# Kernel optimization log

Hardware: AMD Instinct MI355X
Metric: run time of the kernel (lower is better)

The kernel has to match this reference:

```python
import jax, jax.numpy as jnp
import numpy as np

TEMPERATURE = 2.0  # registered buffer in the torch module
TAU = 1.0
N_HEADS = 16


def setup_inputs() -> dict:
    key = jax.random.key(0)
    ks = jax.random.split(key, 8)
    B, S, D, N = 4, 1024, 1024, 4096
    scale = 1.0 / np.sqrt(D)
    return {
        "x": jax.random.normal(ks[0], (B, S, D), jnp.float32),
        "in_proj_w": jax.random.normal(ks[1], (3 * D, D), jnp.float32) * scale,
        "in_proj_b": jnp.zeros((3 * D,), jnp.float32),
        "out_w": jax.random.normal(ks[2], (D, D), jnp.float32) * scale,
        "out_b": jnp.zeros((D,), jnp.float32),
        "aff_w": jax.random.normal(ks[3], (N, D), jnp.float32) * scale,
        "aff_b": jnp.zeros((N,), jnp.float32),
        "k": 256,
    }


def _forward(x, in_proj_w, in_proj_b, out_w, out_b, aff_w, aff_b, k):
    B, S, D = x.shape
    H = N_HEADS
    hd = D // H
    # packed QKV projection (torch nn.MultiheadAttention layout)
    qkv = x @ in_proj_w.T + in_proj_b                      # [B,S,3D]
    q, kk, v = jnp.split(qkv, 3, axis=-1)
    q = q.reshape(B, S, H, hd).transpose(0, 2, 1, 3)       # [B,H,S,hd]
    kk = kk.reshape(B, S, H, hd).transpose(0, 2, 1, 3)
    v = v.reshape(B, S, H, hd).transpose(0, 2, 1, 3)
    scores = jnp.einsum("bhqd,bhkd->bhqk", q, kk) / np.sqrt(hd)
    attn = jax.nn.softmax(scores, axis=-1)                 # [B,H,S,S]
    ctx = jnp.einsum("bhqk,bhkd->bhqd", attn, v)
    ctx = ctx.transpose(0, 2, 1, 3).reshape(B, S, D)
    context = ctx @ out_w.T + out_b                        # [B,S,D]
    # neuron affinity -> max-pool over sequence
    affinity = context @ aff_w.T + aff_b                   # [B,S,N]
    pooled = affinity.max(axis=1)                          # [B,N]
    logits = pooled / TEMPERATURE
    # eval path of gumbel-softmax-topk: plain softmax(logits / tau)
    soft = jax.nn.softmax(logits / TAU, axis=-1)
    _, idx = jax.lax.top_k(logits, k)                      # [B,k]
    mask = jnp.zeros_like(soft).at[jnp.arange(soft.shape[0])[:, None], idx].set(1.0)
    masked = soft * mask
    weights = masked / (masked.sum(axis=-1, keepdims=True) + 1e-8)
    return idx, weights, context


def reference(x, in_proj_w, in_proj_b, out_w, out_b, aff_w, aff_b, k):
    return _forward(x, in_proj_w, in_proj_b, out_w, out_b, aff_w, aff_b, k)
```

## Files before the change

### kernel.cpp

```cpp
#include <hip/hip_runtime.h>
#include <math.h>

namespace {

constexpr int Bb = 4, Ss = 1024, Dd = 1024, Hh = 16, HDim = 64, Nn = 4096;
constexpr int Mm = Bb * Ss;

template <int MODE, int TM>
__global__ __launch_bounds__(256, 2) void gemm_f32(
    const float* __restrict__ A, const float* __restrict__ W,
    const float* __restrict__ bias, float* __restrict__ C, const int K,
    const int ldc) {
  constexpr int BM = TM * 16;
  __shared__ float As[2][16][BM];
  __shared__ float Ws[2][16][128];
  __shared__ float red[2][128];
  const int tid = threadIdx.x;
  const int lane = tid & 63, wv = tid >> 6;
  const int wm = wv >> 1, wn = wv & 1;
  const int lty = lane >> 3, ltx = lane & 7;
  const int m0 = blockIdx.y * BM, n0 = blockIdx.x * 128;
  const int row0 = wm * (BM / 2) + lty * TM;
  const int col0 = wn * 64 + ltx * 8;
  const int asrow = (TM == 8) ? (tid >> 1) : (tid >> 2);
  const int asoff = (TM == 8) ? ((tid & 1) * 8) : ((tid & 3) * 4);
  const int bsrow = tid >> 1, bsoff = (tid & 1) * 8;
  const float* Ap = A + (size_t)(m0 + asrow) * K + asoff;
  const float* Wp = W + (size_t)(n0 + bsrow) * K + bsoff;

  float4 a0r, a1r, w0r, w1r;
  a0r = *(const float4*)(Ap);
  if constexpr (TM == 8) a1r = *(const float4*)(Ap + 4);
  w0r = *(const float4*)(Wp);
  w1r = *(const float4*)(Wp + 4);

  float acc[TM][8] = {};
  const int NT = K / 16;
#pragma unroll 1
  for (int kt = 0; kt < NT; ++kt) {
    float* Ab = &As[kt & 1][0][0];
    float* Wb = &Ws[kt & 1][0][0];
    Ab[(asoff + 0) * BM + asrow] = a0r.x;
    Ab[(asoff + 1) * BM + asrow] = a0r.y;
    Ab[(asoff + 2) * BM + asrow] = a0r.z;
    Ab[(asoff + 3) * BM + asrow] = a0r.w;
    if constexpr (TM == 8) {
      Ab[(asoff + 4) * BM + asrow] = a1r.x;
      Ab[(asoff + 5) * BM + asrow] = a1r.y;
      Ab[(asoff + 6) * BM + asrow] = a1r.z;
      Ab[(asoff + 7) * BM + asrow] = a1r.w;
    }
    Wb[(bsoff + 0) * 128 + bsrow] = w0r.x;
    Wb[(bsoff + 1) * 128 + bsrow] = w0r.y;
    Wb[(bsoff + 2) * 128 + bsrow] = w0r.z;
    Wb[(bsoff + 3) * 128 + bsrow] = w0r.w;
    Wb[(bsoff + 4) * 128 + bsrow] = w1r.x;
    Wb[(bsoff + 5) * 128 + bsrow] = w1r.y;
    Wb[(bsoff + 6) * 128 + bsrow] = w1r.z;
    Wb[(bsoff + 7) * 128 + bsrow] = w1r.w;
    __syncthreads();
    if (kt + 1 < NT) {
      const int kb = (kt + 1) * 16;
      a0r = *(const float4*)(Ap + kb);
      if constexpr (TM == 8) a1r = *(const float4*)(Ap + kb + 4);
      w0r = *(const float4*)(Wp + kb);
      w1r = *(const float4*)(Wp + kb + 4);
    }
#pragma unroll
    for (int kk = 0; kk < 16; ++kk) {
      float4 aq0 = *(const float4*)&Ab[kk * BM + row0];
      float4 aq1;
      if constexpr (TM == 8) aq1 = *(const float4*)&Ab[kk * BM + row0 + 4];
      float4 bq0 = *(const float4*)&Wb[kk * 128 + col0];
      float4 bq1 = *(const float4*)&Wb[kk * 128 + col0 + 4];
      float av[TM];
      av[0] = aq0.x; av[1] = aq0.y; av[2] = aq0.z; av[3] = aq0.w;
      if constexpr (TM == 8) {
        av[4] = aq1.x; av[5] = aq1.y; av[6] = aq1.z; av[7] = aq1.w;
      }
      const float bv[8] = {bq0.x, bq0.y, bq0.z, bq0.w,
                           bq1.x, bq1.y, bq1.z, bq1.w};
#pragma unroll
      for (int i = 0; i < TM; ++i)
#pragma unroll
        for (int j = 0; j < 8; ++j)
          acc[i][j] = fmaf(av[i], bv[j], acc[i][j]);
    }
  }

  if constexpr (MODE == 0) {
    float4 bb0 = *(const float4*)&bias[n0 + col0];
    float4 bb1 = *(const float4*)&bias[n0 + col0 + 4];
    const float bvv[8] = {bb0.x, bb0.y, bb0.z, bb0.w,
                          bb1.x, bb1.y, bb1.z, bb1.w};
#pragma unroll
    for (int i = 0; i < TM; ++i) {
      float* crow = C + (size_t)(m0 + row0 + i) * ldc + n0 + col0;
      float4 o0 = {acc[i][0] + bvv[0], acc[i][1] + bvv[1],
                   acc[i][2] + bvv[2], acc[i][3] + bvv[3]};
      float4 o1 = {acc[i][4] + bvv[4], acc[i][5] + bvv[5],
                   acc[i][6] + bvv[6], acc[i][7] + bvv[7]};
      *(float4*)(crow) = o0;
      *(float4*)(crow + 4) = o1;
    }
  } else {
    float cm[8];
#pragma unroll
    for (int j = 0; j < 8; ++j) {
      float m = acc[0][j];
#pragma unroll
      for (int i = 1; i < TM; ++i) m = fmaxf(m, acc[i][j]);
      m = fmaxf(m, __shfl_xor(m, 8));
      m = fmaxf(m, __shfl_xor(m, 16));
      m = fmaxf(m, __shfl_xor(m, 32));
      cm[j] = m;
    }
    __syncthreads();
    if (lty == 0) {
      float4 c0 = {cm[0], cm[1], cm[2], cm[3]};
      float4 c1 = {cm[4], cm[5], cm[6], cm[7]};
      *(float4*)&red[wm][wn * 64 + ltx * 8] = c0;
      *(float4*)&red[wm][wn * 64 + ltx * 8 + 4] = c1;
    }
    __syncthreads();
    if (tid < 128)
      C[(size_t)blockIdx.y * ldc + n0 + tid] =
          fmaxf(red[0][tid], red[1][tid]);
  }
}

__device__ __forceinline__ int swz(int r, int c) {
  return c ^ ((((r >> 3) ^ r) & 7) << 2);
}

__global__ __launch_bounds__(64, 1) void attn_kernel(
    const float* __restrict__ qkv, float* __restrict__ ctx) {
  __shared__ float Qs[64][64];
  __shared__ float KP[32 * 64];
  __shared__ float Vs[32][64];
  const int lane = threadIdx.x;
  const int rg = lane >> 3, cg = lane & 7;
  const int id = blockIdx.x;
  const int qt = id >> 6, bh = id & 63;
  const int b = bh >> 4, h = bh & 15;
  const int q0 = qt * 64;
  const size_t rstride = 3 * Dd;
  const float* qb = qkv + (size_t)b * Ss * rstride + h * HDim;
  const float* kb_ = qb + Dd;
  const float* vb_ = qb + 2 * Dd;
  {
    const float* qr = qb + (size_t)(q0 + lane) * rstride;
#pragma unroll
    for (int c = 0; c < 64; c += 4)
      *(float4*)&Qs[lane][swz(lane, c)] = *(const float4*)(qr + c);
  }
  const int krow = lane >> 1, khalf = (lane & 1) * 32;
  float4 kreg[8], vreg[8];
  {
    const float* kp = kb_ + (size_t)krow * rstride + khalf;
    const float* vp = vb_ + (size_t)krow * rstride + khalf;
#pragma unroll
    for (int c = 0; c < 8; ++c) {
      kreg[c] = *(const float4*)(kp + 4 * c);
      vreg[c] = *(const float4*)(vp + 4 * c);
    }
  }
  float O[8][8] = {};
  float mr[8], lr[8];
#pragma unroll
  for (int i = 0; i < 8; ++i) { mr[i] = -INFINITY; lr[i] = 0.f; }

#pragma unroll 1
  for (int kt = 0; kt < Ss; kt += 32) {
#pragma unroll
    for (int c = 0; c < 8; ++c) {
      *(float4*)&KP[krow * 64 + swz(krow, khalf + 4 * c)] = kreg[c];
      *(float4*)&Vs[krow][swz(krow, khalf + 4 * c)] = vreg[c];
    }
    if (kt + 32 < Ss) {
      const float* kp = kb_ + (size_t)(kt + 32 + krow) * rstride + khalf;
      const float* vp = vb_ + (size_t)(kt + 32 + krow) * rstride + khalf;
#pragma unroll
      for (int c = 0; c < 8; ++c) {
        kreg[c] = *(const float4*)(kp + 4 * c);
        vreg[c] = *(const float4*)(vp + 4 * c);
      }
    }
    float sc[8][4] = {};
#pragma unroll
    for (int d0 = 0; d0 < HDim; d0 += 4) {
      float4 qa[8], kv[4];
#pragma unroll
      for (int i = 0; i < 8; ++i) {
        const int r = rg * 8 + i;
        qa[i] = *(const float4*)&Qs[r][swz(r, d0)];
      }
#pragma unroll
      for (int j = 0; j < 4; ++j) {
        const int r = cg * 4 + j;
        kv[j] = *(const float4*)&KP[r * 64 + swz(r, d0)];
      }
#pragma unroll
      for (int i = 0; i < 8; ++i)
#pragma unroll
        for (int j = 0; j < 4; ++j) {
          sc[i][j] = fmaf(qa[i].x, kv[j].x, sc[i][j]);
          sc[i][j] = fmaf(qa[i].y, kv[j].y, sc[i][j]);
          sc[i][j] = fmaf(qa[i].z, kv[j].z, sc[i][j]);
          sc[i][j] = fmaf(qa[i].w, kv[j].w, sc[i][j]);
        }
    }
#pragma unroll
    for (int i = 0; i < 8; ++i) {
      const float s0 = sc[i][0] * 0.125f, s1 = sc[i][1] * 0.125f;
      const float s2 = sc[i][2] * 0.125f, s3 = sc[i][3] * 0.125f;
      float tm = fmaxf(fmaxf(s0, s1), fmaxf(s2, s3));
      tm = fmaxf(tm, __shfl_xor(tm, 1));
      tm = fmaxf(tm, __shfl_xor(tm, 2));
      tm = fmaxf(tm, __shfl_xor(tm, 4));
      const float mnew = fmaxf(mr[i], tm);
      const float p0 = __expf(s0 - mnew), p1 = __expf(s1 - mnew);
      const float p2 = __expf(s2 - mnew), p3 = __expf(s3 - mnew);
      float rs = p0 + p1 + p2 + p3;
      rs += __shfl_xor(rs, 1);
      rs += __shfl_xor(rs, 2);
      rs += __shfl_xor(rs, 4);
      const float corr = __expf(mr[i] - mnew);
      lr[i] = lr[i] * corr + rs;
      mr[i] = mnew;
#pragma unroll
      for (int c = 0; c < 8; ++c) O[i][c] *= corr;
      const int r = rg * 8 + i;
      float4 pv = {p0, p1, p2, p3};
      *(float4*)&KP[r * 32 + swz(r, cg * 4)] = pv;
    }
#pragma unroll
    for (int k0 = 0; k0 < 32; k0 += 4) {
      float4 pa[8];
#pragma unroll
      for (int i = 0; i < 8; ++i) {
        const int r = rg * 8 + i;
        pa[i] = *(const float4*)&KP[r * 32 + swz(r, k0)];
      }
#pragma unroll
      for (int jj = 0; jj < 4; ++jj) {
        const int vr = k0 + jj;
        const float4 v0 = *(const float4*)&Vs[vr][swz(vr, cg * 8)];
        const float4 v1 = *(const float4*)&Vs[vr][swz(vr, cg * 8 + 4)];
#pragma unroll
        for (int i = 0; i < 8; ++i) {
          const float p = (jj == 0) ? pa[i].x
                          : (jj == 1) ? pa[i].y
                          : (jj == 2) ? pa[i].z : pa[i].w;
          O[i][0] = fmaf(p, v0.x, O[i][0]);
          O[i][1] = fmaf(p, v0.y, O[i][1]);
          O[i][2] = fmaf(p, v0.z, O[i][2]);
          O[i][3] = fmaf(p, v0.w, O[i][3]);
          O[i][4] = fmaf(p, v1.x, O[i][4]);
          O[i][5] = fmaf(p, v1.y, O[i][5]);
          O[i][6] = fmaf(p, v1.z, O[i][6]);
          O[i][7] = fmaf(p, v1.w, O[i][7]);
        }
      }
    }
  }
#pragma unroll
  for (int i = 0; i < 8; ++i) {
    const float inv = 1.0f / lr[i];
    float* orow =
        ctx + ((size_t)(b * Ss + q0 + rg * 8 + i)) * Dd + h * HDim + cg * 8;
    float4 o0 = {O[i][0] * inv, O[i][1] * inv, O[i][2] * inv, O[i][3] * inv};
    float4 o1 = {O[i][4] * inv, O[i][5] * inv, O[i][6] * inv, O[i][7] * inv};
    *(float4*)(orow) = o0;
    *(float4*)(orow + 4) = o1;
  }
}

__device__ inline unsigned int f2s(float f) {
  unsigned int u = __float_as_uint(f);
  return (u >> 31) ? ~u : (u | 0x80000000u);
}
__device__ inline float s2f(unsigned int s) {
  unsigned int u = (s >> 31) ? (s & 0x7fffffffu) : ~s;
  return __uint_as_float(u);
}

__global__ __launch_bounds__(256) void router_kernel(
    const float* __restrict__ partial, const float* __restrict__ aff_b,
    const int* __restrict__ kp, float* __restrict__ out, int out_size) {
  __shared__ unsigned long long keys[Nn];
  __shared__ float lorig[Nn];
  __shared__ float rv[4];
  const int tid = threadIdx.x;
  const int b = blockIdx.x;
  const int kcount = *kp;
  float* idx_out = out;
  float* w_out = out + (out_size - Mm * Dd - Bb * Nn);
  for (int n = tid; n < Nn; n += 256) {
    float m = partial[(size_t)(b * 8) * Nn + n];
#pragma unroll
    for (int t = 1; t < 8; ++t)
      m = fmaxf(m, partial[(size_t)(b * 8 + t) * Nn + n]);
    float lg = (m + aff_b[n]) * 0.5f;
    lorig[n] = lg;
    keys[n] = ((unsigned long long)f2s(lg) << 32) | (unsigned int)(Nn - 1 - n);
  }
  __syncthreads();
  for (int kk = 2; kk <= Nn; kk <<= 1) {
    for (int j = kk >> 1; j > 0; j >>= 1) {
#pragma unroll 4
      for (int t = tid; t < Nn / 2; t += 256) {
        const int i = 2 * j * (t / j) + (t % j);
        const int p = i + j;
        const bool desc = ((i & kk) == 0);
        unsigned long long a = keys[i], c = keys[p];
        if (desc ? (a < c) : (a > c)) { keys[i] = c; keys[p] = a; }
      }
      __syncthreads();
    }
  }
  const float gm = s2f((unsigned int)(keys[0] >> 32));
  float se = 0.f;
  for (int n = tid; n < Nn; n += 256) se += expf(lorig[n] - gm);
#pragma unroll
  for (int msk = 1; msk < 64; msk <<= 1) se += __shfl_xor(se, msk);
  if ((tid & 63) == 0) rv[tid >> 6] = se;
  __syncthreads();
  se = rv[0] + rv[1] + rv[2] + rv[3];
  __syncthreads();
  float es = 0.f;
  for (int p = tid; p < kcount; p += 256)
    es += expf(s2f((unsigned int)(keys[p] >> 32)) - gm);
#pragma unroll
  for (int msk = 1; msk < 64; msk <<= 1) es += __shfl_xor(es, msk);
  if ((tid & 63) == 0) rv[tid >> 6] = es;
  __syncthreads();
  es = rv[0] + rv[1] + rv[2] + rv[3];
  const float wd = es / se + 1e-8f;
  for (int n = tid; n < Nn; n += 256) w_out[(size_t)b * Nn + n] = 0.f;
  __syncthreads();
  for (int p = tid; p < kcount; p += 256) {
    const unsigned long long kkey = keys[p];
    const int n = Nn - 1 - (int)(kkey & 0xffffffffu);
    const float val = s2f((unsigned int)(kkey >> 32));
    idx_out[b * kcount + p] = (float)n;
    w_out[(size_t)b * Nn + n] = (expf(val - gm) / se) / wd;
  }
}

}

extern "C" void kernel_launch(void* const* d_in, const int* in_sizes, int n_in,
                              void* d_out, int out_size, void* d_ws,
                              size_t ws_size, hipStream_t stream) {
  (void)in_sizes; (void)n_in; (void)ws_size;
  const float* x = (const float*)d_in[0];
  const float* in_proj_w = (const float*)d_in[1];
  const float* in_proj_b = (const float*)d_in[2];
  const float* out_w = (const float*)d_in[3];
  const float* out_b = (const float*)d_in[4];
  const float* aff_w = (const float*)d_in[5];
  const float* aff_b = (const float*)d_in[6];
  const int* kp = (const int*)d_in[7];

  float* qkv = (float*)d_ws;
  float* ctxws = qkv + (size_t)Mm * 3 * Dd;
  float* partial = ctxws + (size_t)Mm * Dd;

  float* out = (float*)d_out;
  float* ctx_out = out + ((size_t)out_size - (size_t)Mm * Dd);

  gemm_f32<0, 8><<<dim3(3 * Dd / 128, Mm / 128), 256, 0, stream>>>(
      x, in_proj_w, in_proj_b, qkv, Dd, 3 * Dd);
  attn_kernel<<<dim3(Ss / 64 * Bb * Hh), 64, 0, stream>>>(qkv, ctxws);
  gemm_f32<0, 4><<<dim3(Dd / 128, Mm / 64), 256, 0, stream>>>(
      ctxws, out_w, out_b, ctx_out, Dd, Dd);
  gemm_f32<2, 8><<<dim3(Nn / 128, Mm / 128), 256, 0, stream>>>(
      ctx_out, aff_w, nullptr, partial, Dd, Nn);
  router_kernel<<<dim3(Bb), 256, 0, stream>>>(partial, aff_b, kp, out, out_size);
}
```

Baseline: 1.512 ms.

## Restructure attention into 4-wave blocks with shared double-buffered K/V via global_load_lds

The attention kernel moves from one 64-thread block per 64-query tile to 256-thread blocks, where each of four waves owns 32 queries and all waves share K/V tiles of 16 keys. Those tiles are double-buffered in LDS and filled with direct global-to-LDS loads, so register staging goes away and K/V traffic is amortised across four waves. The aim is better occupancy and latency hiding in what is probably the dominant kernel. In exchange there is a block-wide barrier every 16 keys and less register blocking per thread (4x2 scores instead of 8x4), which lowers the compute-to-LDS-load ratio.

```diff
diff --git a/kernel.cpp b/kernel.cpp
--- a/kernel.cpp
+++ b/kernel.cpp
@@ -5,6 +5,12 @@
 
 constexpr int Bb = 4, Ss = 1024, Dd = 1024, Hh = 16, HDim = 64, Nn = 4096;
 constexpr int Mm = Bb * Ss;
+
+__device__ inline void gload_lds16(const void* g, void* l) {
+  __builtin_amdgcn_global_load_lds(
+      (const __attribute__((address_space(1))) void*)g,
+      (__attribute__((address_space(3))) void*)l, 16, 0, 0);
+}
 
 template <int MODE, int TM>
 __global__ __launch_bounds__(256, 2) void gemm_f32(
@@ -129,81 +135,84 @@
   }
 }
 
-__device__ __forceinline__ int swz(int r, int c) {
-  return c ^ ((((r >> 3) ^ r) & 7) << 2);
-}
-
-__global__ __launch_bounds__(64, 1) void attn_kernel(
+__device__ __forceinline__ int kkey(int r) { return ((r >> 3) ^ r) & 7; }
+__device__ __forceinline__ int swz(int r, int c) { return c ^ (kkey(r) << 2); }
+__device__ __forceinline__ int swzp(int r, int c) {
+  return c ^ ((kkey(r) & 3) << 2);
+}
+
+__global__ __launch_bounds__(256, 2) void attn_kernel(
     const float* __restrict__ qkv, float* __restrict__ ctx) {
-  __shared__ float Qs[64][64];
-  __shared__ float KP[32 * 64];
-  __shared__ float Vs[32][64];
-  const int lane = threadIdx.x;
+  __shared__ float Qs[4][32][64];
+  __shared__ float Ks[2][16][64];
+  __shared__ float Vs[2][16][64];
+  __shared__ float Pw[4][32][16];
+  const int tid = threadIdx.x, wv = tid >> 6, lane = tid & 63;
   const int rg = lane >> 3, cg = lane & 7;
   const int id = blockIdx.x;
-  const int qt = id >> 6, bh = id & 63;
+  const int qb = id >> 6, bh = id & 63;
   const int b = bh >> 4, h = bh & 15;
-  const int q0 = qt * 64;
+  const int q0 = qb * 128 + wv * 32;
   const size_t rstride = 3 * Dd;
-  const float* qb = qkv + (size_t)b * Ss * rstride + h * HDim;
-  const float* kb_ = qb + Dd;
-  const float* vb_ = qb + 2 * Dd;
+  const float* qbp = qkv + (size_t)b * Ss * rstride + h * HDim;
+  const float* kbp = qbp + Dd;
+  const float* vbp = qbp + 2 * Dd;
+
   {
-    const float* qr = qb + (size_t)(q0 + lane) * rstride;
-#pragma unroll
-    for (int c = 0; c < 64; c += 4)
-      *(float4*)&Qs[lane][swz(lane, c)] = *(const float4*)(qr + c);
-  }
-  const int krow = lane >> 1, khalf = (lane & 1) * 32;
-  float4 kreg[8], vreg[8];
-  {
-    const float* kp = kb_ + (size_t)krow * rstride + khalf;
-    const float* vp = vb_ + (size_t)krow * rstride + khalf;
-#pragma unroll
-    for (int c = 0; c < 8; ++c) {
-      kreg[c] = *(const float4*)(kp + 4 * c);
-      vreg[c] = *(const float4*)(vp + 4 * c);
-    }
-  }
-  float O[8][8] = {};
-  float mr[8], lr[8];
-#pragma unroll
-  for (int i = 0; i < 8; ++i) { mr[i] = -INFINITY; lr[i] = 0.f; }
+    const int r = lane >> 1, ch = (lane & 1) * 32;
+    const float* qr = qbp + (size_t)(q0 + r) * rstride + ch;
+#pragma unroll
+    for (int c = 0; c < 32; c += 4)
+      *(float4*)&Qs[wv][r][swz(r, ch + c)] = *(const float4*)(qr + c);
+  }
+
+  const int srow = lane >> 4;
+  const int scol = (lane & 15) * 4;
+#define STAGE_KV(KT, BF)                                                      \
+  {                                                                           \
+    _Pragma("unroll") for (int j = 0; j < 2; ++j) {                           \
+      const int g = wv * 2 + j;                                               \
+      const int rr = (g & 3) * 4 + srow;                                      \
+      const int cc = swz(rr, scol);                                           \
+      if (g < 4)                                                              \
+        gload_lds16(kbp + (size_t)((KT) + rr) * rstride + cc,                 \
+                    &Ks[BF][(g & 3) * 4][0]);                                 \
+      else                                                                    \
+        gload_lds16(vbp + (size_t)((KT) + rr) * rstride + cc,                 \
+                    &Vs[BF][(g & 3) * 4][0]);                                 \
+    }                                                                         \
+  }
+
+  STAGE_KV(0, 0);
+  __syncthreads();
+
+  float O[4][8] = {};
+  float mr[4], lr[4];
+#pragma unroll
+  for (int i = 0; i < 4; ++i) { mr[i] = -INFINITY; lr[i] = 0.f; }
 
 #pragma unroll 1
-  for (int kt = 0; kt < Ss; kt += 32) {
-#pragma unroll
-    for (int c = 0; c < 8; ++c) {
-      *(float4*)&KP[krow * 64 + swz(krow, khalf + 4 * c)] = kreg[c];
-      *(float4*)&Vs[krow][swz(krow, khalf + 4 * c)] = vreg[c];
-    }
-    if (kt + 32 < Ss) {
-      const float* kp = kb_ + (size_t)(kt + 32 + krow) * rstride + khalf;
-      const float* vp = vb_ + (size_t)(kt + 32 + krow) * rstride + khalf;
-#pragma unroll
-      for (int c = 0; c < 8; ++c) {
-        kreg[c] = *(const float4*)(kp + 4 * c);
-        vreg[c] = *(const float4*)(vp + 4 * c);
-      }
-    }
-    float sc[8][4] = {};
+  for (int t = 0; t < Ss / 16; ++t) {
+    const int cur = t & 1;
+    if (t + 1 < Ss / 16) STAGE_KV((t + 1) * 16, cur ^ 1);
+    float sc[4][2] = {};
 #pragma unroll
     for (int d0 = 0; d0 < HDim; d0 += 4) {
-      float4 qa[8], kv[4];
-#pragma unroll
-      for (int i = 0; i < 8; ++i) {
-        const int r = rg * 8 + i;
-        qa[i] = *(const float4*)&Qs[r][swz(r, d0)];
-      }
-#pragma unroll
-      for (int j = 0; j < 4; ++j) {
-        const int r = cg * 4 + j;
-        kv[j] = *(const float4*)&KP[r * 64 + swz(r, d0)];
-      }
-#pragma unroll
-      for (int i = 0; i < 8; ++i)
-#pragma unroll
-        for (int j = 0; j < 4; ++j) {
+      float4 qa[4], kv[2];
+#pragma unroll
+      for (int i = 0; i < 4; ++i) {
+        const int r = rg * 4 + i;
+        qa[i] = *(const float4*)&Qs[wv][r][swz(r, d0)];
+      }
+#pragma unroll
+      for (int j = 0; j < 2; ++j) {
+        const int r = cg * 2 + j;
+        kv[j] = *(const float4*)&Ks[cur][r][swz(r, d0)];
+      }
+#pragma unroll
+      for (int i = 0; i < 4; ++i)
+#pragma unroll
+        for (int j = 0; j < 2; ++j) {
           sc[i][j] = fmaf(qa[i].x, kv[j].x, sc[i][j]);
           sc[i][j] = fmaf(qa[i].y, kv[j].y, sc[i][j]);
           sc[i][j] = fmaf(qa[i].z, kv[j].z, sc[i][j]);
@@ -211,17 +220,15 @@
         }
     }
 #pragma unroll
-    for (int i = 0; i < 8; ++i) {
+    for (int i = 0; i < 4; ++i) {
       const float s0 = sc[i][0] * 0.125f, s1 = sc[i][1] * 0.125f;
-      const float s2 = sc[i][2] * 0.125f, s3 = sc[i][3] * 0.125f;
-      float tm = fmaxf(fmaxf(s0, s1), fmaxf(s2, s3));
+      float tm = fmaxf(s0, s1);
       tm = fmaxf(tm, __shfl_xor(tm, 1));
       tm = fmaxf(tm, __shfl_xor(tm, 2));
       tm = fmaxf(tm, __shfl_xor(tm, 4));
       const float mnew = fmaxf(mr[i], tm);
       const float p0 = __expf(s0 - mnew), p1 = __expf(s1 - mnew);
-      const float p2 = __expf(s2 - mnew), p3 = __expf(s3 - mnew);
-      float rs = p0 + p1 + p2 + p3;
+      float rs = p0 + p1;
       rs += __shfl_xor(rs, 1);
       rs += __shfl_xor(rs, 2);
       rs += __shfl_xor(rs, 4);
@@ -230,25 +237,25 @@
       mr[i] = mnew;
 #pragma unroll
       for (int c = 0; c < 8; ++c) O[i][c] *= corr;
-      const int r = rg * 8 + i;
-      float4 pv = {p0, p1, p2, p3};
-      *(float4*)&KP[r * 32 + swz(r, cg * 4)] = pv;
-    }
-#pragma unroll
-    for (int k0 = 0; k0 < 32; k0 += 4) {
-      float4 pa[8];
-#pragma unroll
-      for (int i = 0; i < 8; ++i) {
-        const int r = rg * 8 + i;
-        pa[i] = *(const float4*)&KP[r * 32 + swz(r, k0)];
+      const int r = rg * 4 + i;
+      float2 pv = {p0, p1};
+      *(float2*)&Pw[wv][r][swzp(r, cg * 2)] = pv;
+    }
+#pragma unroll
+    for (int k0 = 0; k0 < 16; k0 += 4) {
+      float4 pa[4];
+#pragma unroll
+      for (int i = 0; i < 4; ++i) {
+        const int r = rg * 4 + i;
+        pa[i] = *(const float4*)&Pw[wv][r][swzp(r, k0)];
       }
 #pragma unroll
       for (int jj = 0; jj < 4; ++jj) {
         const int vr = k0 + jj;
-        const float4 v0 = *(const float4*)&Vs[vr][swz(vr, cg * 8)];
-        const float4 v1 = *(const float4*)&Vs[vr][swz(vr, cg * 8 + 4)];
-#pragma unroll
-        for (int i = 0; i < 8; ++i) {
+        const float4 v0 = *(const float4*)&Vs[cur][vr][swz(vr, cg * 8)];
+        const float4 v1 = *(const float4*)&Vs[cur][vr][swz(vr, cg * 8 + 4)];
+#pragma unroll
+        for (int i = 0; i < 4; ++i) {
           const float p = (jj == 0) ? pa[i].x
                           : (jj == 1) ? pa[i].y
                           : (jj == 2) ? pa[i].z : pa[i].w;
@@ -263,17 +270,19 @@
         }
       }
     }
-  }
-#pragma unroll
-  for (int i = 0; i < 8; ++i) {
+    __syncthreads();
+  }
+#pragma unroll
+  for (int i = 0; i < 4; ++i) {
     const float inv = 1.0f / lr[i];
     float* orow =
-        ctx + ((size_t)(b * Ss + q0 + rg * 8 + i)) * Dd + h * HDim + cg * 8;
+        ctx + ((size_t)(b * Ss + q0 + rg * 4 + i)) * Dd + h * HDim + cg * 8;
     float4 o0 = {O[i][0] * inv, O[i][1] * inv, O[i][2] * inv, O[i][3] * inv};
     float4 o1 = {O[i][4] * inv, O[i][5] * inv, O[i][6] * inv, O[i][7] * inv};
     *(float4*)(orow) = o0;
     *(float4*)(orow + 4) = o1;
   }
+#undef STAGE_KV
 }
 
 __device__ inline unsigned int f2s(float f) {
@@ -340,9 +349,9 @@
   for (int n = tid; n < Nn; n += 256) w_out[(size_t)b * Nn + n] = 0.f;
   __syncthreads();
   for (int p = tid; p < kcount; p += 256) {
-    const unsigned long long kkey = keys[p];
-    const int n = Nn - 1 - (int)(kkey & 0xffffffffu);
-    const float val = s2f((unsigned int)(kkey >> 32));
+    const unsigned long long kkey2 = keys[p];
+    const int n = Nn - 1 - (int)(kkey2 & 0xffffffffu);
+    const float val = s2f((unsigned int)(kkey2 >> 32));
     idx_out[b * kcount + p] = (float)n;
     w_out[(size_t)b * Nn + n] = (expf(val - gm) / se) / wd;
   }
@@ -372,7 +381,7 @@
 
   gemm_f32<0, 8><<<dim3(3 * Dd / 128, Mm / 128), 256, 0, stream>>>(
       x, in_proj_w, in_proj_b, qkv, Dd, 3 * Dd);
-  attn_kernel<<<dim3(Ss / 64 * Bb * Hh), 64, 0, stream>>>(qkv, ctxws);
+  attn_kernel<<<dim3(Ss / 128 * Bb * Hh), 256, 0, stream>>>(qkv, ctxws);
   gemm_f32<0, 4><<<dim3(Dd / 128, Mm / 64), 256, 0, stream>>>(
       ctxws, out_w, out_b, ctx_out, Dd, Dd);
   gemm_f32<2, 8><<<dim3(Nn / 128, Mm / 128), 256, 0, stream>>>(
```

Result: faster. 1.262 ms (-16.5%).
